# Kernel tuning notes

Hardware: AMD Instinct MI355X
Metric: run time of the kernel (lower is better)

The kernel has to match this reference:

```python
import jax, jax.numpy as jnp
import numpy as np

B, S, H, L = 64, 512, 768, 32  # batch, seq_len, bert hidden, clauses per doc


def setup_inputs() -> dict:
    key = jax.random.key(0)
    k1, k2, k3, k4 = jax.random.split(key, 4)
    sequence_output = jax.random.normal(k1, (B, S, H), jnp.float32)
    context_h = jax.random.normal(k2, (B, H), jnp.float32)
    # clause boundary positions (SEP indices); pos[0]=0, evenly spaced clauses
    step = (S - 2) // L  # 15 tokens per clause, pos[L]=480 < S-1
    clauses_positions = jnp.tile(jnp.arange(L + 1, dtype=jnp.int32) * step, (B, 1))
    doc_lens = jnp.full((B,), L, dtype=jnp.int32)
    D = 2 * H  # 1536: [clause_mean ; CLS]
    W_pool = jax.random.normal(k3, (D, D), jnp.float32) / np.sqrt(D).astype(np.float32)
    b_pool = jnp.zeros((D,), jnp.float32)
    W_out = jax.random.normal(k4, (D,), jnp.float32) / np.sqrt(D).astype(np.float32)
    b_out = jnp.zeros((), jnp.float32)
    return dict(sequence_output=sequence_output, context_h=context_h,
                W_pool=W_pool, b_pool=b_pool, W_out=W_out, b_out=b_out,
                clauses_positions=clauses_positions, doc_lens=doc_lens)


def reference(sequence_output, context_h, W_pool, b_pool, W_out, b_out,
              clauses_positions, doc_lens):
    # clause i (1..L) covers tokens [pos[i-1]+1, pos[i]]; last clause also
    # includes pos[L]+1 (split_size[-1] += 1 in the torch code).
    starts = clauses_positions[:, :-1] + 1           # [B, L]
    ends = clauses_positions[:, 1:] + 1              # exclusive
    ends = ends.at[:, -1].add(1)                     # last clause gets the SEP
    t = jnp.arange(sequence_output.shape[1])         # [S]
    seg_mask = ((t[None, None, :] >= starts[:, :, None]) &
                (t[None, None, :] < ends[:, :, None]))          # [B, L, S]
    counts = (ends - starts).astype(sequence_output.dtype)      # [B, L]
    sums = jnp.einsum('bls,bsh->blh', seg_mask.astype(sequence_output.dtype),
                      sequence_output)                          # segment sums
    means = sums / counts[:, :, None]                           # [B, L, H]
    cls = jnp.broadcast_to(sequence_output[:, :1, :], means.shape)
    clause_h = jnp.concatenate([means, cls], axis=-1)           # [B, L, 2H]
    pooled = jnp.tanh(clause_h @ W_pool.T + b_pool)             # Pooler
    logits = pooled @ W_out + b_out                             # [B, L]
    return logits
```

## Files before the change

kernel.cpp:

```cpp
#include <hip/hip_runtime.h>
#include <hip/hip_bf16.h>

#define SS 512
#define HH 768
#define LL 32
#define DD 1536
#define MM 2048
#define KK DD

typedef float f32x4 __attribute__((ext_vector_type(4)));
typedef short bf16x8 __attribute__((ext_vector_type(8)));

__device__ __forceinline__ unsigned short f2bf(float x) {
    union { float f; unsigned u; } v; v.f = x;
    unsigned r = v.u + 0x7fff + ((v.u >> 16) & 1);
    return (unsigned short)(r >> 16);
}

__device__ __forceinline__ void gload16(const unsigned short* g, unsigned short* l) {
    __builtin_amdgcn_global_load_lds(
        (const __attribute__((address_space(1))) void*)g,
        (__attribute__((address_space(3))) void*)l, 16, 0, 0);
}

__global__ __launch_bounds__(256)
void prep(const float* __restrict__ seq, const int* __restrict__ pos,
          const float* __restrict__ Wp, const float* __restrict__ bo,
          unsigned short* __restrict__ Abf, unsigned short* __restrict__ Wbf,
          float* __restrict__ out) {
    int blk = blockIdx.x;
    int tid = threadIdx.x;
    if (blk < MM) {
        int b = blk >> 5;
        int l = blk & 31;
        const int* pb = pos + b * (LL + 1);
        int start = pb[l] + 1;
        int end   = pb[l + 1] + 1;
        if (l == LL - 1) end += 1;
        float inv = 1.0f / (float)(end - start);
        const float* base = seq + (size_t)b * SS * HH;
        float a0 = 0.f, a1 = 0.f, a2 = 0.f;
        for (int t = start; t < end; ++t) {
            const float* p = base + (size_t)t * HH;
            a0 += p[tid]; a1 += p[tid + 256]; a2 += p[tid + 512];
        }
        unsigned short* o = Abf + (size_t)blk * DD;
        o[tid]       = f2bf(a0 * inv);
        o[tid + 256] = f2bf(a1 * inv);
        o[tid + 512] = f2bf(a2 * inv);
        o[HH + tid]       = f2bf(base[tid]);
        o[HH + tid + 256] = f2bf(base[tid + 256]);
        o[HH + tid + 512] = f2bf(base[tid + 512]);
    } else if (blk < MM + (DD * DD / 1024)) {
        int i = ((blk - MM) * 256 + tid) * 4;
        float4 v = *(const float4*)(Wp + i);
        ushort4 o;
        o.x = f2bf(v.x); o.y = f2bf(v.y); o.z = f2bf(v.z); o.w = f2bf(v.w);
        *(ushort4*)(Wbf + i) = o;
    } else {
        int i = (blk - MM - DD * DD / 1024) * 256 + tid;
        if (i < MM) out[i] = bo[0];
    }
}

__global__ __launch_bounds__(256, 3)
void gemm_mfma(const unsigned short* __restrict__ A,
               const unsigned short* __restrict__ Bm,
               const float* __restrict__ bp,
               const float* __restrict__ Wo,
               float* __restrict__ out) {
    __shared__ unsigned short As[3 * 4096];
    __shared__ unsigned short Bs[3 * 4096];
    const int tid  = threadIdx.x;
    const int wid  = tid >> 6;
    const int lane = tid & 63;
    const int fr   = lane & 15;
    const int fq   = lane >> 4;
    const int wr   = wid >> 1, wc = wid & 1;

    const int blk = blockIdx.x;
    const int c = blk & 7;
    const int i = blk >> 3;
    const int bm = ((c >> 1) << 3) + (i & 7);
    const int bn = (c & 1) * 12 + (i >> 3);
    const int brow = bm * 64;
    const int bcol = bn * 64;

    const int srow = tid >> 3;
    const int sc   = (tid & 7) ^ (srow & 7);
    const unsigned short* gA = A  + (size_t)(brow + srow) * KK + sc * 8;
    const unsigned short* gB = Bm + (size_t)(bcol + srow) * KK + sc * 8;
    unsigned short* asW = As + wid * 512;
    unsigned short* bsW = Bs + wid * 512;

#define STAGE(buf, kt) do {                                          \
        gload16(gA + (kt) * 64,           asW + (buf) * 4096);       \
        gload16(gA + (kt) * 64 + 32 * KK, asW + (buf) * 4096 + 2048);\
        gload16(gB + (kt) * 64,           bsW + (buf) * 4096);       \
        gload16(gB + (kt) * 64 + 32 * KK, bsW + (buf) * 4096 + 2048);\
    } while (0)

    const int s0 = fq ^ (fr & 7);
    const int s1 = s0 ^ 4;
    const int rA = wr * 32 + fr;
    const int rB = wc * 32 + fr;
    const int oA00 = rA * 64 + s0 * 8, oA01 = rA * 64 + s1 * 8;
    const int oA10 = oA00 + 16 * 64,   oA11 = oA01 + 16 * 64;
    const int oB00 = rB * 64 + s0 * 8, oB01 = rB * 64 + s1 * 8;
    const int oB10 = oB00 + 16 * 64,   oB11 = oB01 + 16 * 64;

    f32x4 acc[2][2] = {};

    STAGE(0, 0); STAGE(1, 1); STAGE(2, 2);

#define BODY(t, buf) do {                                                     \
        __builtin_amdgcn_sched_barrier(0);                                    \
        if ((t) <= 21)      asm volatile("s_waitcnt vmcnt(8)" ::: "memory");  \
        else if ((t) == 22) asm volatile("s_waitcnt vmcnt(4)" ::: "memory");  \
        else                asm volatile("s_waitcnt vmcnt(0)" ::: "memory");  \
        __builtin_amdgcn_s_barrier();                                         \
        const unsigned short* as_ = As + (buf) * 4096;                        \
        const unsigned short* bs_ = Bs + (buf) * 4096;                        \
        bf16x8 a00 = *(const bf16x8*)(as_ + oA00);                            \
        bf16x8 a01 = *(const bf16x8*)(as_ + oA01);                            \
        bf16x8 a10 = *(const bf16x8*)(as_ + oA10);                            \
        bf16x8 a11 = *(const bf16x8*)(as_ + oA11);                            \
        bf16x8 b00 = *(const bf16x8*)(bs_ + oB00);                            \
        bf16x8 b01 = *(const bf16x8*)(bs_ + oB01);                            \
        bf16x8 b10 = *(const bf16x8*)(bs_ + oB10);                            \
        bf16x8 b11 = *(const bf16x8*)(bs_ + oB11);                            \
        asm volatile("s_waitcnt lgkmcnt(0)" ::: "memory");                    \
        __builtin_amdgcn_s_barrier();                                         \
        if ((t) + 3 < 24) STAGE(buf, (t) + 3);                                \
        acc[0][0] = __builtin_amdgcn_mfma_f32_16x16x32_bf16(a00, b00, acc[0][0], 0, 0, 0); \
        acc[0][0] = __builtin_amdgcn_mfma_f32_16x16x32_bf16(a01, b01, acc[0][0], 0, 0, 0); \
        acc[0][1] = __builtin_amdgcn_mfma_f32_16x16x32_bf16(a00, b10, acc[0][1], 0, 0, 0); \
        acc[0][1] = __builtin_amdgcn_mfma_f32_16x16x32_bf16(a01, b11, acc[0][1], 0, 0, 0); \
        acc[1][0] = __builtin_amdgcn_mfma_f32_16x16x32_bf16(a10, b00, acc[1][0], 0, 0, 0); \
        acc[1][0] = __builtin_amdgcn_mfma_f32_16x16x32_bf16(a11, b01, acc[1][0], 0, 0, 0); \
        acc[1][1] = __builtin_amdgcn_mfma_f32_16x16x32_bf16(a10, b10, acc[1][1], 0, 0, 0); \
        acc[1][1] = __builtin_amdgcn_mfma_f32_16x16x32_bf16(a11, b11, acc[1][1], 0, 0, 0); \
    } while (0)

    #pragma unroll
    for (int t = 0; t < 24; ++t) {
        BODY(t, t % 3);
    }
#undef BODY
#undef STAGE

    #pragma unroll
    for (int m = 0; m < 2; ++m) {
        float vsum[4] = {0.f, 0.f, 0.f, 0.f};
        #pragma unroll
        for (int n = 0; n < 2; ++n) {
            const int col = bcol + wc * 32 + n * 16 + fr;
            const float wo_ = Wo[col];
            const float pb_ = bp[col];
            #pragma unroll
            for (int r = 0; r < 4; ++r) {
                float x = acc[m][n][r] + pb_;
                float th = 1.f - 2.f / (__expf(2.f * x) + 1.f);
                vsum[r] += th * wo_;
            }
        }
        #pragma unroll
        for (int r = 0; r < 4; ++r) {
            float v = vsum[r];
            v += __shfl_xor(v, 1, 16);
            v += __shfl_xor(v, 2, 16);
            v += __shfl_xor(v, 4, 16);
            v += __shfl_xor(v, 8, 16);
            if (fr == 0)
                atomicAdd(&out[brow + wr * 32 + m * 16 + fq * 4 + r], v);
        }
    }
}

extern "C" void kernel_launch(void* const* d_in, const int* in_sizes, int n_in,
                              void* d_out, int out_size, void* d_ws, size_t ws_size,
                              hipStream_t stream) {
    const float* seq   = (const float*)d_in[0];
    const float* Wp    = (const float*)d_in[2];
    const float* bp    = (const float*)d_in[3];
    const float* Wo    = (const float*)d_in[4];
    const float* bo    = (const float*)d_in[5];
    const int*   pos   = (const int*)d_in[6];
    float* out = (float*)d_out;

    unsigned short* Abf = (unsigned short*)d_ws;
    unsigned short* Wbf = Abf + (size_t)MM * DD;

    const int nconv = DD * DD / 1024;
    const int ninit = (MM + 255) / 256;
    prep<<<MM + nconv + ninit, 256, 0, stream>>>(seq, pos, Wp, bo, Abf, Wbf, out);
    gemm_mfma<<<768, 256, 0, stream>>>(Abf, Wbf, bp, Wo, out);
}
```

Before: 41.34 us.

## Replace four-wave GEMM block with single-wave 64x64 tile without barriers

The GEMM block shrinks from four waves, each computing a 32x32 sub-tile, to a single wave that computes the whole 64x64 output tile with a 4x4 grid of MFMA accumulators. With only one wave per block, the s_barrier synchronisation is gone. Prefetch distance drops to two stages over three LDS buffers, and LDS fragment loads for the second K-half are interleaved with the MFMAs. The aim is to cut barrier overhead and raise per-wave register reuse of A/B fragments, at the cost of far fewer resident waves per CU and less latency hiding.

```diff
diff --git a/kernel.cpp b/kernel.cpp
--- a/kernel.cpp
+++ b/kernel.cpp
@@ -63,83 +63,94 @@
     }
 }
 
-__global__ __launch_bounds__(256, 3)
-void gemm_mfma(const unsigned short* __restrict__ A,
-               const unsigned short* __restrict__ Bm,
-               const float* __restrict__ bp,
-               const float* __restrict__ Wo,
-               float* __restrict__ out) {
+__global__ __launch_bounds__(64)
+void gemm64(const unsigned short* __restrict__ A,
+            const unsigned short* __restrict__ Bm,
+            const float* __restrict__ bp,
+            const float* __restrict__ Wo,
+            float* __restrict__ out) {
     __shared__ unsigned short As[3 * 4096];
     __shared__ unsigned short Bs[3 * 4096];
-    const int tid  = threadIdx.x;
-    const int wid  = tid >> 6;
-    const int lane = tid & 63;
+    const int lane = threadIdx.x;
     const int fr   = lane & 15;
     const int fq   = lane >> 4;
-    const int wr   = wid >> 1, wc = wid & 1;
 
     const int blk = blockIdx.x;
-    const int c = blk & 7;
-    const int i = blk >> 3;
-    const int bm = ((c >> 1) << 3) + (i & 7);
-    const int bn = (c & 1) * 12 + (i >> 3);
+    const int c  = blk & 7;
+    const int ii = blk >> 3;
+    const int bm = ((c >> 1) << 3) + (ii & 7);
+    const int bn = (c & 1) * 12 + (ii >> 3);
     const int brow = bm * 64;
     const int bcol = bn * 64;
 
-    const int srow = tid >> 3;
-    const int sc   = (tid & 7) ^ (srow & 7);
-    const unsigned short* gA = A  + (size_t)(brow + srow) * KK + sc * 8;
-    const unsigned short* gB = Bm + (size_t)(bcol + srow) * KK + sc * 8;
-    unsigned short* asW = As + wid * 512;
-    unsigned short* bsW = Bs + wid * 512;
-
-#define STAGE(buf, kt) do {                                          \
-        gload16(gA + (kt) * 64,           asW + (buf) * 4096);       \
-        gload16(gA + (kt) * 64 + 32 * KK, asW + (buf) * 4096 + 2048);\
-        gload16(gB + (kt) * 64,           bsW + (buf) * 4096);       \
-        gload16(gB + (kt) * 64 + 32 * KK, bsW + (buf) * 4096 + 2048);\
+    const int srow = lane >> 3;
+    const int sch  = (lane & 7) ^ srow;
+    const unsigned short* gA = A  + (size_t)(brow + srow) * KK + sch * 8;
+    const unsigned short* gB = Bm + (size_t)(bcol + srow) * KK + sch * 8;
+
+#define STAGE(buf, t) do {                                                    \
+        _Pragma("unroll")                                                     \
+        for (int s8 = 0; s8 < 8; ++s8) {                                      \
+            gload16(gA + (size_t)s8 * 8 * KK + (t) * 64,                      \
+                    As + (buf) * 4096 + s8 * 512);                            \
+            gload16(gB + (size_t)s8 * 8 * KK + (t) * 64,                      \
+                    Bs + (buf) * 4096 + s8 * 512);                            \
+        }                                                                     \
     } while (0)
 
-    const int s0 = fq ^ (fr & 7);
-    const int s1 = s0 ^ 4;
-    const int rA = wr * 32 + fr;
-    const int rB = wc * 32 + fr;
-    const int oA00 = rA * 64 + s0 * 8, oA01 = rA * 64 + s1 * 8;
-    const int oA10 = oA00 + 16 * 64,   oA11 = oA01 + 16 * 64;
-    const int oB00 = rB * 64 + s0 * 8, oB01 = rB * 64 + s1 * 8;
-    const int oB10 = oB00 + 16 * 64,   oB11 = oB01 + 16 * 64;
-
-    f32x4 acc[2][2] = {};
-
-    STAGE(0, 0); STAGE(1, 1); STAGE(2, 2);
+    const int sl0 = fq ^ (fr & 7);
+    const int oA0 = fr * 64 + sl0 * 8;
+    const int oA1 = fr * 64 + (sl0 ^ 4) * 8;
+
+    f32x4 acc[4][4] = {};
+
+    STAGE(0, 0); STAGE(1, 1);
+
+#define MFMA_HALF(A0, A1, A2, A3, B0, B1, B2, B3) do {                        \
+        acc[0][0] = __builtin_amdgcn_mfma_f32_16x16x32_bf16(A0, B0, acc[0][0], 0, 0, 0); \
+        acc[0][1] = __builtin_amdgcn_mfma_f32_16x16x32_bf16(A0, B1, acc[0][1], 0, 0, 0); \
+        acc[0][2] = __builtin_amdgcn_mfma_f32_16x16x32_bf16(A0, B2, acc[0][2], 0, 0, 0); \
+        acc[0][3] = __builtin_amdgcn_mfma_f32_16x16x32_bf16(A0, B3, acc[0][3], 0, 0, 0); \
+        acc[1][0] = __builtin_amdgcn_mfma_f32_16x16x32_bf16(A1, B0, acc[1][0], 0, 0, 0); \
+        acc[1][1] = __builtin_amdgcn_mfma_f32_16x16x32_bf16(A1, B1, acc[1][1], 0, 0, 0); \
+        acc[1][2] = __builtin_amdgcn_mfma_f32_16x16x32_bf16(A1, B2, acc[1][2], 0, 0, 0); \
+        acc[1][3] = __builtin_amdgcn_mfma_f32_16x16x32_bf16(A1, B3, acc[1][3], 0, 0, 0); \
+        acc[2][0] = __builtin_amdgcn_mfma_f32_16x16x32_bf16(A2, B0, acc[2][0], 0, 0, 0); \
+        acc[2][1] = __builtin_amdgcn_mfma_f32_16x16x32_bf16(A2, B1, acc[2][1], 0, 0, 0); \
+        acc[2][2] = __builtin_amdgcn_mfma_f32_16x16x32_bf16(A2, B2, acc[2][2], 0, 0, 0); \
+        acc[2][3] = __builtin_amdgcn_mfma_f32_16x16x32_bf16(A2, B3, acc[2][3], 0, 0, 0); \
+        acc[3][0] = __builtin_amdgcn_mfma_f32_16x16x32_bf16(A3, B0, acc[3][0], 0, 0, 0); \
+        acc[3][1] = __builtin_amdgcn_mfma_f32_16x16x32_bf16(A3, B1, acc[3][1], 0, 0, 0); \
+        acc[3][2] = __builtin_amdgcn_mfma_f32_16x16x32_bf16(A3, B2, acc[3][2], 0, 0, 0); \
+        acc[3][3] = __builtin_amdgcn_mfma_f32_16x16x32_bf16(A3, B3, acc[3][3], 0, 0, 0); \
+    } while (0)
 
 #define BODY(t, buf) do {                                                     \
         __builtin_amdgcn_sched_barrier(0);                                    \
-        if ((t) <= 21)      asm volatile("s_waitcnt vmcnt(8)" ::: "memory");  \
-        else if ((t) == 22) asm volatile("s_waitcnt vmcnt(4)" ::: "memory");  \
-        else                asm volatile("s_waitcnt vmcnt(0)" ::: "memory");  \
-        __builtin_amdgcn_s_barrier();                                         \
+        if ((t) <= 22) asm volatile("s_waitcnt vmcnt(16)" ::: "memory");      \
+        else           asm volatile("s_waitcnt vmcnt(0)"  ::: "memory");      \
+        __builtin_amdgcn_sched_barrier(0);                                    \
         const unsigned short* as_ = As + (buf) * 4096;                        \
         const unsigned short* bs_ = Bs + (buf) * 4096;                        \
-        bf16x8 a00 = *(const bf16x8*)(as_ + oA00);                            \
-        bf16x8 a01 = *(const bf16x8*)(as_ + oA01);                            \
-        bf16x8 a10 = *(const bf16x8*)(as_ + oA10);                            \
-        bf16x8 a11 = *(const bf16x8*)(as_ + oA11);                            \
-        bf16x8 b00 = *(const bf16x8*)(bs_ + oB00);                            \
-        bf16x8 b01 = *(const bf16x8*)(bs_ + oB01);                            \
-        bf16x8 b10 = *(const bf16x8*)(bs_ + oB10);                            \
-        bf16x8 b11 = *(const bf16x8*)(bs_ + oB11);                            \
-        asm volatile("s_waitcnt lgkmcnt(0)" ::: "memory");                    \
-        __builtin_amdgcn_s_barrier();                                         \
-        if ((t) + 3 < 24) STAGE(buf, (t) + 3);                                \
-        acc[0][0] = __builtin_amdgcn_mfma_f32_16x16x32_bf16(a00, b00, acc[0][0], 0, 0, 0); \
-        acc[0][0] = __builtin_amdgcn_mfma_f32_16x16x32_bf16(a01, b01, acc[0][0], 0, 0, 0); \
-        acc[0][1] = __builtin_amdgcn_mfma_f32_16x16x32_bf16(a00, b10, acc[0][1], 0, 0, 0); \
-        acc[0][1] = __builtin_amdgcn_mfma_f32_16x16x32_bf16(a01, b11, acc[0][1], 0, 0, 0); \
-        acc[1][0] = __builtin_amdgcn_mfma_f32_16x16x32_bf16(a10, b00, acc[1][0], 0, 0, 0); \
-        acc[1][0] = __builtin_amdgcn_mfma_f32_16x16x32_bf16(a11, b01, acc[1][0], 0, 0, 0); \
-        acc[1][1] = __builtin_amdgcn_mfma_f32_16x16x32_bf16(a10, b10, acc[1][1], 0, 0, 0); \
-        acc[1][1] = __builtin_amdgcn_mfma_f32_16x16x32_bf16(a11, b11, acc[1][1], 0, 0, 0); \
+        bf16x8 a0 = *(const bf16x8*)(as_ + oA0);                              \
+        bf16x8 a1 = *(const bf16x8*)(as_ + oA0 + 1024);                       \
+        bf16x8 a2 = *(const bf16x8*)(as_ + oA0 + 2048);                       \
+        bf16x8 a3 = *(const bf16x8*)(as_ + oA0 + 3072);                       \
+        bf16x8 b0 = *(const bf16x8*)(bs_ + oA0);                              \
+        bf16x8 b1 = *(const bf16x8*)(bs_ + oA0 + 1024);                       \
+        bf16x8 b2 = *(const bf16x8*)(bs_ + oA0 + 2048);                       \
+        bf16x8 b3 = *(const bf16x8*)(bs_ + oA0 + 3072);                       \
+        if ((t) + 2 < 24) STAGE(((t) + 2) % 3, (t) + 2);                      \
+        MFMA_HALF(a0, a1, a2, a3, b0, b1, b2, b3);                            \
+        a0 = *(const bf16x8*)(as_ + oA1);                                     \
+        a1 = *(const bf16x8*)(as_ + oA1 + 1024);                              \
+        a2 = *(const bf16x8*)(as_ + oA1 + 2048);                              \
+        a3 = *(const bf16x8*)(as_ + oA1 + 3072);                              \
+        b0 = *(const bf16x8*)(bs_ + oA1);                                     \
+        b1 = *(const bf16x8*)(bs_ + oA1 + 1024);                              \
+        b2 = *(const bf16x8*)(bs_ + oA1 + 2048);                              \
+        b3 = *(const bf16x8*)(bs_ + oA1 + 3072);                              \
+        MFMA_HALF(a0, a1, a2, a3, b0, b1, b2, b3);                            \
     } while (0)
 
     #pragma unroll
@@ -147,14 +158,15 @@
         BODY(t, t % 3);
     }
 #undef BODY
+#undef MFMA_HALF
 #undef STAGE
 
     #pragma unroll
-    for (int m = 0; m < 2; ++m) {
+    for (int m = 0; m < 4; ++m) {
         float vsum[4] = {0.f, 0.f, 0.f, 0.f};
         #pragma unroll
-        for (int n = 0; n < 2; ++n) {
-            const int col = bcol + wc * 32 + n * 16 + fr;
+        for (int n = 0; n < 4; ++n) {
+            const int col = bcol + n * 16 + fr;
             const float wo_ = Wo[col];
             const float pb_ = bp[col];
             #pragma unroll
@@ -172,7 +184,7 @@
             v += __shfl_xor(v, 4, 16);
             v += __shfl_xor(v, 8, 16);
             if (fr == 0)
-                atomicAdd(&out[brow + wr * 32 + m * 16 + fq * 4 + r], v);
+                atomicAdd(&out[brow + m * 16 + fq * 4 + r], v);
         }
     }
 }
@@ -194,5 +206,5 @@
     const int nconv = DD * DD / 1024;
     const int ninit = (MM + 255) / 256;
     prep<<<MM + nconv + ninit, 256, 0, stream>>>(seq, pos, Wp, bo, Abf, Wbf, out);
-    gemm_mfma<<<768, 256, 0, stream>>>(Abf, Wbf, bp, Wo, out);
-}
+    gemm64<<<768, 64, 0, stream>>>(Abf, Wbf, bp, Wo, out);
+}
```

Measured after the change: 46.41 us. 1.12x slower.

## Vectorize prep with 192-thread float4 blocks and single-barrier GEMM pipeline

Applied to the files above, without the earlier changes.

The prep kernel now runs 192 threads per block, each handling a float4 of the 768-wide hidden dimension. This vectorizes the segment-sum loads and the bf16 stores, and the block counts for the weight conversion and output init are rescaled to match. The GEMM main loop drops from two barriers per K-step to one. It prefetches stage t+2 right after the barrier at a looser vmcnt, and raises wave priority around the MFMA block. This cuts sync overhead and instruction count, at the cost of a shallower prefetch distance (two tiles ahead instead of three).

```diff
diff --git a/kernel.cpp b/kernel.cpp
--- a/kernel.cpp
+++ b/kernel.cpp
@@ -23,13 +23,13 @@
         (__attribute__((address_space(3))) void*)l, 16, 0, 0);
 }
 
-__global__ __launch_bounds__(256)
+__global__ __launch_bounds__(192)
 void prep(const float* __restrict__ seq, const int* __restrict__ pos,
           const float* __restrict__ Wp, const float* __restrict__ bo,
           unsigned short* __restrict__ Abf, unsigned short* __restrict__ Wbf,
           float* __restrict__ out) {
-    int blk = blockIdx.x;
-    int tid = threadIdx.x;
+    const int blk = blockIdx.x;
+    const int tid = threadIdx.x;
     if (blk < MM) {
         int b = blk >> 5;
         int l = blk & 31;
@@ -39,26 +39,28 @@
         if (l == LL - 1) end += 1;
         float inv = 1.0f / (float)(end - start);
         const float* base = seq + (size_t)b * SS * HH;
-        float a0 = 0.f, a1 = 0.f, a2 = 0.f;
+        float4 a = make_float4(0.f, 0.f, 0.f, 0.f);
         for (int t = start; t < end; ++t) {
-            const float* p = base + (size_t)t * HH;
-            a0 += p[tid]; a1 += p[tid + 256]; a2 += p[tid + 512];
+            float4 v = reinterpret_cast<const float4*>(base + (size_t)t * HH)[tid];
+            a.x += v.x; a.y += v.y; a.z += v.z; a.w += v.w;
         }
         unsigned short* o = Abf + (size_t)blk * DD;
-        o[tid]       = f2bf(a0 * inv);
-        o[tid + 256] = f2bf(a1 * inv);
-        o[tid + 512] = f2bf(a2 * inv);
-        o[HH + tid]       = f2bf(base[tid]);
-        o[HH + tid + 256] = f2bf(base[tid + 256]);
-        o[HH + tid + 512] = f2bf(base[tid + 512]);
-    } else if (blk < MM + (DD * DD / 1024)) {
-        int i = ((blk - MM) * 256 + tid) * 4;
+        ushort4 m;
+        m.x = f2bf(a.x * inv); m.y = f2bf(a.y * inv);
+        m.z = f2bf(a.z * inv); m.w = f2bf(a.w * inv);
+        reinterpret_cast<ushort4*>(o)[tid] = m;
+        float4 c = reinterpret_cast<const float4*>(base)[tid];
+        ushort4 cc;
+        cc.x = f2bf(c.x); cc.y = f2bf(c.y); cc.z = f2bf(c.z); cc.w = f2bf(c.w);
+        reinterpret_cast<ushort4*>(o + HH)[tid] = cc;
+    } else if (blk < MM + 3072) {
+        int i = ((blk - MM) * 192 + tid) * 4;
         float4 v = *(const float4*)(Wp + i);
         ushort4 o;
         o.x = f2bf(v.x); o.y = f2bf(v.y); o.z = f2bf(v.z); o.w = f2bf(v.w);
         *(ushort4*)(Wbf + i) = o;
     } else {
-        int i = (blk - MM - DD * DD / 1024) * 256 + tid;
+        int i = (blk - MM - 3072) * 192 + tid;
         if (i < MM) out[i] = bo[0];
     }
 }
@@ -111,14 +113,15 @@
 
     f32x4 acc[2][2] = {};
 
-    STAGE(0, 0); STAGE(1, 1); STAGE(2, 2);
+    STAGE(0, 0); STAGE(1, 1);
 
 #define BODY(t, buf) do {                                                     \
         __builtin_amdgcn_sched_barrier(0);                                    \
-        if ((t) <= 21)      asm volatile("s_waitcnt vmcnt(8)" ::: "memory");  \
-        else if ((t) == 22) asm volatile("s_waitcnt vmcnt(4)" ::: "memory");  \
-        else                asm volatile("s_waitcnt vmcnt(0)" ::: "memory");  \
+        if ((t) <= 22) asm volatile("s_waitcnt vmcnt(4)" ::: "memory");       \
+        else           asm volatile("s_waitcnt vmcnt(0)" ::: "memory");       \
         __builtin_amdgcn_s_barrier();                                         \
+        __builtin_amdgcn_sched_barrier(0);                                    \
+        if ((t) + 2 < 24) STAGE(((t) + 2) % 3, (t) + 2);                      \
         const unsigned short* as_ = As + (buf) * 4096;                        \
         const unsigned short* bs_ = Bs + (buf) * 4096;                        \
         bf16x8 a00 = *(const bf16x8*)(as_ + oA00);                            \
@@ -129,9 +132,7 @@
         bf16x8 b01 = *(const bf16x8*)(bs_ + oB01);                            \
         bf16x8 b10 = *(const bf16x8*)(bs_ + oB10);                            \
         bf16x8 b11 = *(const bf16x8*)(bs_ + oB11);                            \
-        asm volatile("s_waitcnt lgkmcnt(0)" ::: "memory");                    \
-        __builtin_amdgcn_s_barrier();                                         \
-        if ((t) + 3 < 24) STAGE(buf, (t) + 3);                                \
+        __builtin_amdgcn_s_setprio(1);                                        \
         acc[0][0] = __builtin_amdgcn_mfma_f32_16x16x32_bf16(a00, b00, acc[0][0], 0, 0, 0); \
         acc[0][0] = __builtin_amdgcn_mfma_f32_16x16x32_bf16(a01, b01, acc[0][0], 0, 0, 0); \
         acc[0][1] = __builtin_amdgcn_mfma_f32_16x16x32_bf16(a00, b10, acc[0][1], 0, 0, 0); \
@@ -140,6 +141,7 @@
         acc[1][0] = __builtin_amdgcn_mfma_f32_16x16x32_bf16(a11, b01, acc[1][0], 0, 0, 0); \
         acc[1][1] = __builtin_amdgcn_mfma_f32_16x16x32_bf16(a10, b10, acc[1][1], 0, 0, 0); \
         acc[1][1] = __builtin_amdgcn_mfma_f32_16x16x32_bf16(a11, b11, acc[1][1], 0, 0, 0); \
+        __builtin_amdgcn_s_setprio(0);                                        \
     } while (0)
 
     #pragma unroll
@@ -191,8 +193,7 @@
     unsigned short* Abf = (unsigned short*)d_ws;
     unsigned short* Wbf = Abf + (size_t)MM * DD;
 
-    const int nconv = DD * DD / 1024;
-    const int ninit = (MM + 255) / 256;
-    prep<<<MM + nconv + ninit, 256, 0, stream>>>(seq, pos, Wp, bo, Abf, Wbf, out);
+    const int ninit = (MM + 191) / 192;
+    prep<<<MM + 3072 + ninit, 192, 0, stream>>>(seq, pos, Wp, bo, Abf, Wbf, out);
     gemm_mfma<<<768, 256, 0, stream>>>(Abf, Wbf, bp, Wo, out);
 }
```

After: 42.13 us. Within noise of the previous version (+1.9%).

## Factor CLS half of pooler GEMM into per-batch precompute, halve GEMM K

Applied to the files above, without the earlier changes.

The CLS half of each clause row is identical across the 32 clauses of a document, so its product with the right half of W_pool is computed once per batch (64x1536) inside prep and added as a bias in the GEMM epilogue. The main GEMM then runs over K=768 instead of 1536, and the bf16 A and W buffers shrink to 768 columns. The GEMM pipeline is also reworked: two stages in flight, the next stage issued right after the barrier, and s_setprio around the MFMAs. This adds a small, unpipelined GEMM of 24 blocks inside prep, which could become the critical path of that kernel.

```diff
diff --git a/kernel.cpp b/kernel.cpp
--- a/kernel.cpp
+++ b/kernel.cpp
@@ -6,7 +6,8 @@
 #define LL 32
 #define DD 1536
 #define MM 2048
-#define KK DD
+#define KA 768
+#define NSTEP 12
 
 typedef float f32x4 __attribute__((ext_vector_type(4)));
 typedef short bf16x8 __attribute__((ext_vector_type(8)));
@@ -27,12 +28,83 @@
 void prep(const float* __restrict__ seq, const int* __restrict__ pos,
           const float* __restrict__ Wp, const float* __restrict__ bo,
           unsigned short* __restrict__ Abf, unsigned short* __restrict__ Wbf,
-          float* __restrict__ out) {
-    int blk = blockIdx.x;
-    int tid = threadIdx.x;
-    if (blk < MM) {
-        int b = blk >> 5;
-        int l = blk & 31;
+          float* __restrict__ C2, float* __restrict__ out) {
+    __shared__ unsigned short CAs[64 * 64];
+    __shared__ unsigned short CBs[64 * 64];
+    const int blk = blockIdx.x;
+    const int tid = threadIdx.x;
+
+    if (blk < 24) {
+        const int bcol = blk * 64;
+        const int lane = tid & 63;
+        const int wid  = tid >> 6;
+        const int fr = lane & 15, fq = lane >> 4;
+        const int wr = wid >> 1,  wc = wid & 1;
+        const int crow = tid >> 2;
+        const int cf   = tid & 3;
+        const float* gA = seq + (size_t)crow * SS * HH;
+        const float* gW = Wp  + (size_t)(bcol + crow) * DD + HH;
+        const int s0 = fq ^ (fr & 7);
+        const int s1 = s0 ^ 4;
+        const int rA = wr * 32 + fr;
+        const int rB = wc * 32 + fr;
+        const int oA00 = rA * 64 + s0 * 8, oA01 = rA * 64 + s1 * 8;
+        const int oA10 = oA00 + 16 * 64,   oA11 = oA01 + 16 * 64;
+        const int oB00 = rB * 64 + s0 * 8, oB01 = rB * 64 + s1 * 8;
+        const int oB10 = oB00 + 16 * 64,   oB11 = oB01 + 16 * 64;
+
+        f32x4 acc[2][2] = {};
+        for (int t = 0; t < NSTEP; ++t) {
+            const int k0 = t * 64;
+            __syncthreads();
+            #pragma unroll
+            for (int j = 0; j < 4; ++j) {
+                const int f4   = cf + j * 4;
+                const int slot = (f4 >> 1) ^ (crow & 7);
+                const int off  = crow * 64 + slot * 8 + (f4 & 1) * 4;
+                float4 av = *(const float4*)(gA + k0 + f4 * 4);
+                float4 wv = *(const float4*)(gW + k0 + f4 * 4);
+                ushort4 au, wu;
+                au.x = f2bf(av.x); au.y = f2bf(av.y);
+                au.z = f2bf(av.z); au.w = f2bf(av.w);
+                wu.x = f2bf(wv.x); wu.y = f2bf(wv.y);
+                wu.z = f2bf(wv.z); wu.w = f2bf(wv.w);
+                *(ushort4*)&CAs[off] = au;
+                *(ushort4*)&CBs[off] = wu;
+            }
+            __syncthreads();
+            bf16x8 a00 = *(const bf16x8*)&CAs[oA00];
+            bf16x8 a01 = *(const bf16x8*)&CAs[oA01];
+            bf16x8 a10 = *(const bf16x8*)&CAs[oA10];
+            bf16x8 a11 = *(const bf16x8*)&CAs[oA11];
+            bf16x8 b00 = *(const bf16x8*)&CBs[oB00];
+            bf16x8 b01 = *(const bf16x8*)&CBs[oB01];
+            bf16x8 b10 = *(const bf16x8*)&CBs[oB10];
+            bf16x8 b11 = *(const bf16x8*)&CBs[oB11];
+            acc[0][0] = __builtin_amdgcn_mfma_f32_16x16x32_bf16(a00, b00, acc[0][0], 0, 0, 0);
+            acc[0][0] = __builtin_amdgcn_mfma_f32_16x16x32_bf16(a01, b01, acc[0][0], 0, 0, 0);
+            acc[0][1] = __builtin_amdgcn_mfma_f32_16x16x32_bf16(a00, b10, acc[0][1], 0, 0, 0);
+            acc[0][1] = __builtin_amdgcn_mfma_f32_16x16x32_bf16(a01, b11, acc[0][1], 0, 0, 0);
+            acc[1][0] = __builtin_amdgcn_mfma_f32_16x16x32_bf16(a10, b00, acc[1][0], 0, 0, 0);
+            acc[1][0] = __builtin_amdgcn_mfma_f32_16x16x32_bf16(a11, b01, acc[1][0], 0, 0, 0);
+            acc[1][1] = __builtin_amdgcn_mfma_f32_16x16x32_bf16(a10, b10, acc[1][1], 0, 0, 0);
+            acc[1][1] = __builtin_amdgcn_mfma_f32_16x16x32_bf16(a11, b11, acc[1][1], 0, 0, 0);
+        }
+        #pragma unroll
+        for (int m = 0; m < 2; ++m)
+            #pragma unroll
+            for (int n = 0; n < 2; ++n) {
+                const int col = bcol + wc * 32 + n * 16 + fr;
+                #pragma unroll
+                for (int r = 0; r < 4; ++r) {
+                    const int row = wr * 32 + m * 16 + fq * 4 + r;
+                    C2[(size_t)row * DD + col] = acc[m][n][r];
+                }
+            }
+    } else if (blk < 24 + MM) {
+        const int row = blk - 24;
+        const int b = row >> 5;
+        const int l = row & 31;
         const int* pb = pos + b * (LL + 1);
         int start = pb[l] + 1;
         int end   = pb[l + 1] + 1;
@@ -44,21 +116,19 @@
             const float* p = base + (size_t)t * HH;
             a0 += p[tid]; a1 += p[tid + 256]; a2 += p[tid + 512];
         }
-        unsigned short* o = Abf + (size_t)blk * DD;
+        unsigned short* o = Abf + (size_t)row * KA;
         o[tid]       = f2bf(a0 * inv);
         o[tid + 256] = f2bf(a1 * inv);
         o[tid + 512] = f2bf(a2 * inv);
-        o[HH + tid]       = f2bf(base[tid]);
-        o[HH + tid + 256] = f2bf(base[tid + 256]);
-        o[HH + tid + 512] = f2bf(base[tid + 512]);
-    } else if (blk < MM + (DD * DD / 1024)) {
-        int i = ((blk - MM) * 256 + tid) * 4;
-        float4 v = *(const float4*)(Wp + i);
-        ushort4 o;
-        o.x = f2bf(v.x); o.y = f2bf(v.y); o.z = f2bf(v.z); o.w = f2bf(v.w);
-        *(ushort4*)(Wbf + i) = o;
+    } else if (blk < 24 + MM + DD) {
+        const int n = blk - 24 - MM;
+        const float* src = Wp + (size_t)n * DD;
+        unsigned short* dst = Wbf + (size_t)n * KA;
+        dst[tid]       = f2bf(src[tid]);
+        dst[tid + 256] = f2bf(src[tid + 256]);
+        dst[tid + 512] = f2bf(src[tid + 512]);
     } else {
-        int i = (blk - MM - DD * DD / 1024) * 256 + tid;
+        const int i = (blk - 24 - MM - DD) * 256 + tid;
         if (i < MM) out[i] = bo[0];
     }
 }
@@ -66,6 +136,7 @@
 __global__ __launch_bounds__(256, 3)
 void gemm_mfma(const unsigned short* __restrict__ A,
                const unsigned short* __restrict__ Bm,
+               const float* __restrict__ C2g,
                const float* __restrict__ bp,
                const float* __restrict__ Wo,
                float* __restrict__ out) {
@@ -88,16 +159,16 @@
 
     const int srow = tid >> 3;
     const int sc   = (tid & 7) ^ (srow & 7);
-    const unsigned short* gA = A  + (size_t)(brow + srow) * KK + sc * 8;
-    const unsigned short* gB = Bm + (size_t)(bcol + srow) * KK + sc * 8;
+    const unsigned short* gA = A  + (size_t)(brow + srow) * KA + sc * 8;
+    const unsigned short* gB = Bm + (size_t)(bcol + srow) * KA + sc * 8;
     unsigned short* asW = As + wid * 512;
     unsigned short* bsW = Bs + wid * 512;
 
 #define STAGE(buf, kt) do {                                          \
         gload16(gA + (kt) * 64,           asW + (buf) * 4096);       \
-        gload16(gA + (kt) * 64 + 32 * KK, asW + (buf) * 4096 + 2048);\
+        gload16(gA + (kt) * 64 + 32 * KA, asW + (buf) * 4096 + 2048);\
         gload16(gB + (kt) * 64,           bsW + (buf) * 4096);       \
-        gload16(gB + (kt) * 64 + 32 * KK, bsW + (buf) * 4096 + 2048);\
+        gload16(gB + (kt) * 64 + 32 * KA, bsW + (buf) * 4096 + 2048);\
     } while (0)
 
     const int s0 = fq ^ (fr & 7);
@@ -111,14 +182,15 @@
 
     f32x4 acc[2][2] = {};
 
-    STAGE(0, 0); STAGE(1, 1); STAGE(2, 2);
+    STAGE(0, 0); STAGE(1, 1);
 
 #define BODY(t, buf) do {                                                     \
         __builtin_amdgcn_sched_barrier(0);                                    \
-        if ((t) <= 21)      asm volatile("s_waitcnt vmcnt(8)" ::: "memory");  \
-        else if ((t) == 22) asm volatile("s_waitcnt vmcnt(4)" ::: "memory");  \
-        else                asm volatile("s_waitcnt vmcnt(0)" ::: "memory");  \
+        if ((t) < NSTEP - 1) asm volatile("s_waitcnt vmcnt(4)" ::: "memory"); \
+        else                 asm volatile("s_waitcnt vmcnt(0)" ::: "memory"); \
         __builtin_amdgcn_s_barrier();                                         \
+        __builtin_amdgcn_sched_barrier(0);                                    \
+        if ((t) + 2 < NSTEP) STAGE(((t) + 2) % 3, (t) + 2);                   \
         const unsigned short* as_ = As + (buf) * 4096;                        \
         const unsigned short* bs_ = Bs + (buf) * 4096;                        \
         bf16x8 a00 = *(const bf16x8*)(as_ + oA00);                            \
@@ -129,9 +201,7 @@
         bf16x8 b01 = *(const bf16x8*)(bs_ + oB01);                            \
         bf16x8 b10 = *(const bf16x8*)(bs_ + oB10);                            \
         bf16x8 b11 = *(const bf16x8*)(bs_ + oB11);                            \
-        asm volatile("s_waitcnt lgkmcnt(0)" ::: "memory");                    \
-        __builtin_amdgcn_s_barrier();                                         \
-        if ((t) + 3 < 24) STAGE(buf, (t) + 3);                                \
+        __builtin_amdgcn_s_setprio(1);                                        \
         acc[0][0] = __builtin_amdgcn_mfma_f32_16x16x32_bf16(a00, b00, acc[0][0], 0, 0, 0); \
         acc[0][0] = __builtin_amdgcn_mfma_f32_16x16x32_bf16(a01, b01, acc[0][0], 0, 0, 0); \
         acc[0][1] = __builtin_amdgcn_mfma_f32_16x16x32_bf16(a00, b10, acc[0][1], 0, 0, 0); \
@@ -140,28 +210,34 @@
         acc[1][0] = __builtin_amdgcn_mfma_f32_16x16x32_bf16(a11, b01, acc[1][0], 0, 0, 0); \
         acc[1][1] = __builtin_amdgcn_mfma_f32_16x16x32_bf16(a10, b10, acc[1][1], 0, 0, 0); \
         acc[1][1] = __builtin_amdgcn_mfma_f32_16x16x32_bf16(a11, b11, acc[1][1], 0, 0, 0); \
+        __builtin_amdgcn_s_setprio(0);                                        \
     } while (0)
 
     #pragma unroll
-    for (int t = 0; t < 24; ++t) {
+    for (int t = 0; t < NSTEP; ++t) {
         BODY(t, t % 3);
     }
 #undef BODY
 #undef STAGE
 
+    const float* c2row = C2g + (size_t)(2 * bm + wr) * DD;
+    float wo_[2], ad_[2];
+    #pragma unroll
+    for (int n = 0; n < 2; ++n) {
+        const int col = bcol + wc * 32 + n * 16 + fr;
+        wo_[n] = Wo[col];
+        ad_[n] = bp[col] + c2row[col];
+    }
     #pragma unroll
     for (int m = 0; m < 2; ++m) {
         float vsum[4] = {0.f, 0.f, 0.f, 0.f};
         #pragma unroll
         for (int n = 0; n < 2; ++n) {
-            const int col = bcol + wc * 32 + n * 16 + fr;
-            const float wo_ = Wo[col];
-            const float pb_ = bp[col];
             #pragma unroll
             for (int r = 0; r < 4; ++r) {
-                float x = acc[m][n][r] + pb_;
+                float x = acc[m][n][r] + ad_[n];
                 float th = 1.f - 2.f / (__expf(2.f * x) + 1.f);
-                vsum[r] += th * wo_;
+                vsum[r] += th * wo_[n];
             }
         }
         #pragma unroll
@@ -189,10 +265,10 @@
     float* out = (float*)d_out;
 
     unsigned short* Abf = (unsigned short*)d_ws;
-    unsigned short* Wbf = Abf + (size_t)MM * DD;
-
-    const int nconv = DD * DD / 1024;
-    const int ninit = (MM + 255) / 256;
-    prep<<<MM + nconv + ninit, 256, 0, stream>>>(seq, pos, Wp, bo, Abf, Wbf, out);
-    gemm_mfma<<<768, 256, 0, stream>>>(Abf, Wbf, bp, Wo, out);
-}
+    unsigned short* Wbf = Abf + (size_t)MM * KA;
+    float*          C2  = (float*)(Wbf + (size_t)DD * KA);
+
+    const int grid = 24 + MM + DD + (MM + 255) / 256;
+    prep<<<grid, 256, 0, stream>>>(seq, pos, Wp, bo, Abf, Wbf, C2, out);
+    gemm_mfma<<<768, 256, 0, stream>>>(Abf, Wbf, C2, bp, Wo, out);
+}
```

Measured after the change: 38.16 us. -7.7%, faster.
